# Kernel optimization log

Hardware: AMD Instinct MI355X
Metric: run time of the kernel (lower is better)

The kernel has to match this reference:

```python
import jax, jax.numpy as jnp
import numpy as np

N = 262144   # active voxels
C = 128      # channels (in == out, residual requires it)
K = 27       # 3x3x3 kernel offsets
M = 131072   # kernel-map pairs per offset
EPS = 1e-5


def setup_inputs() -> dict:
    key = jax.random.key(0)
    ks = jax.random.split(key, 10)
    feats = jax.random.normal(ks[0], (N, C), dtype=jnp.float32)
    in_maps = jax.random.randint(ks[1], (K, M), 0, N, dtype=jnp.int32)
    out_maps = jax.random.randint(ks[2], (K, M), 0, N, dtype=jnp.int32)
    # conv weights: one [Cin, Cout] matrix per kernel offset (ME layout), no bias
    W1 = jax.random.normal(ks[3], (K, C, C), dtype=jnp.float32) * (1.0 / np.sqrt(C * K))
    W2 = jax.random.normal(ks[4], (K, C, C), dtype=jnp.float32) * (1.0 / np.sqrt(C * K))
    gamma1 = jnp.ones((C,), jnp.float32)
    beta1 = jnp.zeros((C,), jnp.float32)
    gamma2 = jnp.ones((C,), jnp.float32)
    beta2 = jnp.zeros((C,), jnp.float32)
    return {"feats": feats, "in_maps": in_maps, "out_maps": out_maps,
            "W1": W1, "gamma1": gamma1, "beta1": beta1,
            "W2": W2, "gamma2": gamma2, "beta2": beta2}


def sparse_conv(feats, W, in_maps, out_maps):
    # gather-GEMM-scatter over K=27 kernel offsets (stride 1: N_out == N_in)
    out = jnp.zeros((feats.shape[0], W.shape[2]), feats.dtype)
    for k in range(K):
        gathered = feats[in_maps[k]]          # [M, Cin] irregular gather
        contrib = gathered @ W[k]             # [M, Cout] GEMM
        out = out.at[out_maps[k]].add(contrib)  # scatter-add
    return out


def batch_norm(x, gamma, beta):
    # training-mode BN over the voxel dim with batch stats (biased var)
    mean = jnp.mean(x, axis=0)
    var = jnp.mean(jnp.square(x - mean), axis=0)
    return (x - mean) * jax.lax.rsqrt(var + EPS) * gamma + beta


def reference(feats, in_maps, out_maps, W1, gamma1, beta1, W2, gamma2, beta2):
    out = sparse_conv(feats, W1, in_maps, out_maps)
    out = jax.nn.relu(batch_norm(out, gamma1, beta1))
    out = sparse_conv(out, W2, in_maps, out_maps)
    out = batch_norm(out, gamma2, beta2)
    return jax.nn.relu(out + feats)  # downsample=None -> identity residual
```

## Files before the change

kernel.cpp:

```cpp
#include <hip/hip_runtime.h>
#include <cstdint>

typedef __bf16  bf16x8  __attribute__((ext_vector_type(8)));
typedef short   short8v __attribute__((ext_vector_type(8)));
typedef float   f32x4   __attribute__((ext_vector_type(4)));

constexpr int N  = 262144;
constexpr int C  = 128;
constexpr int K  = 27;
constexpr int M  = 131072;
constexpr int BR = 64;
constexpr int TILES_PER_K = M / BR;

__device__ __forceinline__ uint16_t f2bf(float f) {
    union { float f; uint32_t u; } x; x.f = f;
    uint32_t r = (x.u + 0x7FFFu + ((x.u >> 16) & 1u)) >> 16;
    return (uint16_t)r;
}

__global__ __launch_bounds__(256) void cast_feats_kernel(
    const float* __restrict__ in, uint16_t* __restrict__ out) {
    int i = blockIdx.x * 256 + threadIdx.x;
    const float4* src = reinterpret_cast<const float4*>(in) + (size_t)i * 2;
    float4 a = src[0], b = src[1];
    union { uint16_t u[8]; short8v v; } r;
    r.u[0]=f2bf(a.x); r.u[1]=f2bf(a.y); r.u[2]=f2bf(a.z); r.u[3]=f2bf(a.w);
    r.u[4]=f2bf(b.x); r.u[5]=f2bf(b.y); r.u[6]=f2bf(b.z); r.u[7]=f2bf(b.w);
    *(reinterpret_cast<short8v*>(out) + i) = r.v;
}

__global__ __launch_bounds__(256) void transpose_w_kernel(
    const float* __restrict__ W1, const float* __restrict__ W2,
    uint16_t* __restrict__ WT1, uint16_t* __restrict__ WT2) {
    int i = blockIdx.x * 256 + threadIdx.x;
    int k    = i / (C * C);
    int rem  = i - k * (C * C);
    int cout = rem >> 7;
    int cin  = rem & 127;
    int src  = k * C * C + cin * C + cout;
    WT1[i] = f2bf(W1[src]);
    WT2[i] = f2bf(W2[src]);
}

__global__ __launch_bounds__(256, 3) void conv_kernel(
    const uint16_t* __restrict__ featsB,
    const uint16_t* __restrict__ WT,
    const int* __restrict__ in_maps,
    const int* __restrict__ out_maps,
    float* __restrict__ out)
{
    __shared__ char lds[BR * C * 2 + C * C * 2];
    char* Alds = lds;
    char* Wlds = lds + BR * C * 2;

    const int tile = blockIdx.x;
    const int k    = tile / TILES_PER_K;
    const int m0   = (tile % TILES_PER_K) * BR;
    const int tid  = threadIdx.x;

    {
        const int* im = in_maps + k * M + m0;
        #pragma unroll
        for (int i = 0; i < 4; ++i) {
            int chunk = tid + 256 * i;
            int row   = chunk >> 4;
            int c8    = chunk & 15;
            int g     = im[row];
            short8v v = *reinterpret_cast<const short8v*>(featsB + g * C + c8 * 8);
            int off = (row * 256 + c8 * 16) ^ ((row & 7) << 4);
            *reinterpret_cast<short8v*>(Alds + off) = v;
        }
        const uint16_t* w = WT + k * C * C;
        #pragma unroll
        for (int i = 0; i < 8; ++i) {
            int chunk = tid + 256 * i;
            int cout  = chunk >> 4;
            int c8    = chunk & 15;
            short8v v = *reinterpret_cast<const short8v*>(w + chunk * 8);
            int off = (cout * 256 + c8 * 16) ^ ((cout & 7) << 4);
            *reinterpret_cast<short8v*>(Wlds + off) = v;
        }
    }
    __syncthreads();

    const int wave  = tid >> 6;
    const int lane  = tid & 63;
    const int r16   = lane & 15;
    const int khalf = lane >> 4;

    short8v a[4];
    {
        int row  = wave * 16 + r16;
        int base = row * 256;
        int swz  = (row & 7) << 4;
        #pragma unroll
        for (int kk = 0; kk < 4; ++kk)
            a[kk] = *reinterpret_cast<const short8v*>(Alds + ((base + kk * 64 + khalf * 16) ^ swz));
    }

    f32x4 acc[8];
    #pragma unroll
    for (int t = 0; t < 8; ++t) acc[t] = (f32x4){0.f, 0.f, 0.f, 0.f};

    #pragma unroll
    for (int t = 0; t < 8; ++t) {
        int col  = t * 16 + r16;
        int base = col * 256;
        int swz  = (col & 7) << 4;
        #pragma unroll
        for (int kk = 0; kk < 4; ++kk) {
            short8v b = *reinterpret_cast<const short8v*>(Wlds + ((base + kk * 64 + khalf * 16) ^ swz));
            acc[t] = __builtin_amdgcn_mfma_f32_16x16x32_bf16(
                __builtin_bit_cast(bf16x8, a[kk]), __builtin_bit_cast(bf16x8, b), acc[t], 0, 0, 0);
        }
    }

    const int* om = out_maps + k * M + m0 + wave * 16;
    #pragma unroll
    for (int j = 0; j < 4; ++j) {
        int g = om[khalf * 4 + j];
        float* dst = out + g * C + r16;
        #pragma unroll
        for (int t = 0; t < 8; ++t)
            unsafeAtomicAdd(dst + t * 16, acc[t][j]);
    }
}

__global__ __launch_bounds__(256) void stats_kernel(
    const float* __restrict__ x, float* __restrict__ sums) {
    const int tid = threadIdx.x;
    const int c32 = tid & 31;
    const int rg  = tid >> 5;
    constexpr int RPB = N / 1024;
    float4 s = {0,0,0,0}, q = {0,0,0,0};
    const float* base = x + (size_t)blockIdx.x * RPB * C + c32 * 4;
    for (int r = rg; r < RPB; r += 8) {
        float4 v = *reinterpret_cast<const float4*>(base + r * C);
        s.x += v.x; s.y += v.y; s.z += v.z; s.w += v.w;
        q.x += v.x*v.x; q.y += v.y*v.y; q.z += v.z*v.z; q.w += v.w*v.w;
    }
    __shared__ float4 red[8][32];
    red[rg][c32] = s;
    __syncthreads();
    if (rg == 0) {
        float4 t = red[0][c32];
        #pragma unroll
        for (int j = 1; j < 8; ++j) { float4 u = red[j][c32]; t.x+=u.x; t.y+=u.y; t.z+=u.z; t.w+=u.w; }
        unsafeAtomicAdd(&sums[c32*4+0], t.x); unsafeAtomicAdd(&sums[c32*4+1], t.y);
        unsafeAtomicAdd(&sums[c32*4+2], t.z); unsafeAtomicAdd(&sums[c32*4+3], t.w);
    }
    __syncthreads();
    red[rg][c32] = q;
    __syncthreads();
    if (rg == 0) {
        float4 t = red[0][c32];
        #pragma unroll
        for (int j = 1; j < 8; ++j) { float4 u = red[j][c32]; t.x+=u.x; t.y+=u.y; t.z+=u.z; t.w+=u.w; }
        unsafeAtomicAdd(&sums[C+c32*4+0], t.x); unsafeAtomicAdd(&sums[C+c32*4+1], t.y);
        unsafeAtomicAdd(&sums[C+c32*4+2], t.z); unsafeAtomicAdd(&sums[C+c32*4+3], t.w);
    }
}

__global__ void finalize_kernel(const float* __restrict__ sums,
                                const float* __restrict__ gamma, const float* __restrict__ beta,
                                float* __restrict__ ss) {
    int c = threadIdx.x;
    float m  = sums[c] * (1.0f / N);
    float v  = sums[C + c] * (1.0f / N) - m * m;
    float r  = rsqrtf(v + 1e-5f);
    float sc = gamma[c] * r;
    ss[c]     = sc;
    ss[C + c] = beta[c] - m * sc;
}

__global__ __launch_bounds__(256) void bnrelu_kernel(
    const float* __restrict__ x, const float* __restrict__ ss, uint16_t* __restrict__ out) {
    int i = blockIdx.x * 256 + threadIdx.x;
    int base = i * 8;
    int c = base & 127;
    float4 sc0 = *reinterpret_cast<const float4*>(ss + c);
    float4 sc1 = *reinterpret_cast<const float4*>(ss + c + 4);
    float4 sh0 = *reinterpret_cast<const float4*>(ss + C + c);
    float4 sh1 = *reinterpret_cast<const float4*>(ss + C + c + 4);
    const float4* src = reinterpret_cast<const float4*>(x + base);
    float4 a = src[0], b = src[1];
    union { uint16_t u[8]; short8v v; } r;
    r.u[0] = f2bf(fmaxf(fmaf(a.x, sc0.x, sh0.x), 0.f));
    r.u[1] = f2bf(fmaxf(fmaf(a.y, sc0.y, sh0.y), 0.f));
    r.u[2] = f2bf(fmaxf(fmaf(a.z, sc0.z, sh0.z), 0.f));
    r.u[3] = f2bf(fmaxf(fmaf(a.w, sc0.w, sh0.w), 0.f));
    r.u[4] = f2bf(fmaxf(fmaf(b.x, sc1.x, sh1.x), 0.f));
    r.u[5] = f2bf(fmaxf(fmaf(b.y, sc1.y, sh1.y), 0.f));
    r.u[6] = f2bf(fmaxf(fmaf(b.z, sc1.z, sh1.z), 0.f));
    r.u[7] = f2bf(fmaxf(fmaf(b.w, sc1.w, sh1.w), 0.f));
    *(reinterpret_cast<short8v*>(out) + i) = r.v;
}

__global__ __launch_bounds__(256) void final_kernel(
    float* __restrict__ x, const float* __restrict__ feats, const float* __restrict__ ss) {
    int i = blockIdx.x * 256 + threadIdx.x;
    int base = i * 4;
    int c = base & 127;
    float4 sc = *reinterpret_cast<const float4*>(ss + c);
    float4 sh = *reinterpret_cast<const float4*>(ss + C + c);
    float4 v  = *reinterpret_cast<const float4*>(x + base);
    float4 f  = *reinterpret_cast<const float4*>(feats + base);
    float4 o;
    o.x = fmaxf(fmaf(v.x, sc.x, sh.x) + f.x, 0.f);
    o.y = fmaxf(fmaf(v.y, sc.y, sh.y) + f.y, 0.f);
    o.z = fmaxf(fmaf(v.z, sc.z, sh.z) + f.z, 0.f);
    o.w = fmaxf(fmaf(v.w, sc.w, sh.w) + f.w, 0.f);
    *reinterpret_cast<float4*>(x + base) = o;
}

extern "C" void kernel_launch(void* const* d_in, const int* in_sizes, int n_in,
                              void* d_out, int out_size, void* d_ws, size_t ws_size,
                              hipStream_t stream) {
    const float* feats   = (const float*)d_in[0];
    const int* in_maps   = (const int*)d_in[1];
    const int* out_maps  = (const int*)d_in[2];
    const float* W1      = (const float*)d_in[3];
    const float* gamma1  = (const float*)d_in[4];
    const float* beta1   = (const float*)d_in[5];
    const float* W2      = (const float*)d_in[6];
    const float* gamma2  = (const float*)d_in[7];
    const float* beta2   = (const float*)d_in[8];
    float* out = (float*)d_out;

    char* ws = (char*)d_ws;
    uint16_t* featsB = (uint16_t*)(ws);
    uint16_t* bn1B   = (uint16_t*)(ws + 67108864);
    uint16_t* WT1    = (uint16_t*)(ws + 134217728);
    uint16_t* WT2    = (uint16_t*)(ws + 135102464);
    float*    sums1  = (float*)   (ws + 135987200);
    float*    sums2  = sums1 + 256;
    float*    ss1    = sums1 + 512;
    float*    ss2    = sums1 + 768;

    hipMemsetAsync(out, 0, (size_t)N * C * 4, stream);
    hipMemsetAsync(sums1, 0, 512 * 4, stream);

    cast_feats_kernel<<<N * C / 8 / 256, 256, 0, stream>>>(feats, featsB);
    transpose_w_kernel<<<K * C * C / 256, 256, 0, stream>>>(W1, W2, WT1, WT2);

    conv_kernel<<<K * TILES_PER_K, 256, 0, stream>>>(featsB, WT1, in_maps, out_maps, out);
    stats_kernel<<<1024, 256, 0, stream>>>(out, sums1);
    finalize_kernel<<<1, 128, 0, stream>>>(sums1, gamma1, beta1, ss1);
    bnrelu_kernel<<<N * C / 8 / 256, 256, 0, stream>>>(out, ss1, bn1B);

    hipMemsetAsync(out, 0, (size_t)N * C * 4, stream);
    conv_kernel<<<K * TILES_PER_K, 256, 0, stream>>>(bn1B, WT2, in_maps, out_maps, out);
    stats_kernel<<<1024, 256, 0, stream>>>(out, sums2);
    finalize_kernel<<<1, 128, 0, stream>>>(sums2, gamma2, beta2, ss2);
    final_kernel<<<N * C / 4 / 256, 256, 0, stream>>>(out, feats, ss2);
}
```

Baseline: 3.403 ms.

## Replace atomic scatter-add with output-sorted contributions and segmented reduction

Each convolution's fp32 atomic scatter-add into the output is replaced by a deterministic two-pass scheme. A histogram, a three-kernel prefix scan and a scatter kernel build a CSR-style ordering of all kernel-map pairs by output voxel. The GEMM then writes bf16 contributions directly to their sorted slots, and a reduce kernel sums each voxel's segment into the output. This removes per-element global atomics but adds a roughly 900 MB intermediate buffer plus extra write and read traffic, and rounds each contribution to bf16 before accumulation. The new path runs only when the workspace is large enough; otherwise the old path is kept.

After: 3.395 ms. Within noise of the previous version (-0.2%).

```diff
diff --git a/kernel.cpp b/kernel.cpp
--- a/kernel.cpp
+++ b/kernel.cpp
@@ -9,6 +9,7 @@
 constexpr int C  = 128;
 constexpr int K  = 27;
 constexpr int M  = 131072;
+constexpr int KM = K * M;
 constexpr int BR = 64;
 constexpr int TILES_PER_K = M / BR;
 
@@ -16,6 +17,10 @@
     union { float f; uint32_t u; } x; x.f = f;
     uint32_t r = (x.u + 0x7FFFu + ((x.u >> 16) & 1u)) >> 16;
     return (uint16_t)r;
+}
+__device__ __forceinline__ float bf2f(uint16_t u) {
+    union { uint32_t u; float f; } x; x.u = ((uint32_t)u) << 16;
+    return x.f;
 }
 
 __global__ __launch_bounds__(256) void cast_feats_kernel(
@@ -40,6 +45,173 @@
     int src  = k * C * C + cin * C + cout;
     WT1[i] = f2bf(W1[src]);
     WT2[i] = f2bf(W2[src]);
+}
+
+__global__ __launch_bounds__(256) void hist_kernel(
+    const int* __restrict__ out_maps, int* __restrict__ counts) {
+    int i = blockIdx.x * 256 + threadIdx.x;
+    atomicAdd(&counts[out_maps[i]], 1);
+}
+
+__global__ __launch_bounds__(256) void scan1_kernel(
+    const int* __restrict__ counts, int* __restrict__ row_start, int* __restrict__ bsum) {
+    __shared__ int lds[256];
+    int t = threadIdx.x;
+    int base = blockIdx.x * 1024 + t * 4;
+    int4 c = *reinterpret_cast<const int4*>(counts + base);
+    int tot = c.x + c.y + c.z + c.w;
+    lds[t] = tot;
+    __syncthreads();
+    for (int off = 1; off < 256; off <<= 1) {
+        int v = (t >= off) ? lds[t - off] : 0;
+        __syncthreads();
+        lds[t] += v;
+        __syncthreads();
+    }
+    int excl = lds[t] - tot;
+    int4 o;
+    o.x = excl; o.y = excl + c.x; o.z = o.y + c.y; o.w = o.z + c.z;
+    *reinterpret_cast<int4*>(row_start + base) = o;
+    if (t == 255) bsum[blockIdx.x] = lds[255];
+}
+
+__global__ void scan2_kernel(int* __restrict__ bsum) {
+    __shared__ int lds[256];
+    int t = threadIdx.x;
+    int v0 = bsum[t];
+    lds[t] = v0;
+    __syncthreads();
+    for (int off = 1; off < 256; off <<= 1) {
+        int v = (t >= off) ? lds[t - off] : 0;
+        __syncthreads();
+        lds[t] += v;
+        __syncthreads();
+    }
+    bsum[t] = lds[t] - v0;
+}
+
+__global__ __launch_bounds__(256) void scan3_kernel(
+    int* __restrict__ row_start, const int* __restrict__ bsum) {
+    int i = blockIdx.x * 256 + threadIdx.x;
+    row_start[i] += bsum[i >> 10];
+    if (i == 0) row_start[N] = KM;
+}
+
+__global__ __launch_bounds__(256) void scatter_kernel(
+    const int* __restrict__ out_maps, const int* __restrict__ row_start,
+    int* __restrict__ cursor, int* __restrict__ posArr) {
+    int i = blockIdx.x * 256 + threadIdx.x;
+    int o = out_maps[i];
+    int pos = row_start[o] + atomicAdd(&cursor[o], 1);
+    posArr[i] = pos;
+}
+
+__global__ __launch_bounds__(256, 3) void gemm_kernel(
+    const uint16_t* __restrict__ featsB,
+    const uint16_t* __restrict__ WT,
+    const int* __restrict__ in_maps,
+    const int* __restrict__ posArr,
+    uint16_t* __restrict__ contrib)
+{
+    __shared__ char lds[BR * C * 2 + C * C * 2];
+    char* Alds = lds;
+    char* Wlds = lds + BR * C * 2;
+
+    const int tile = blockIdx.x;
+    const int k    = tile / TILES_PER_K;
+    const int m0   = (tile % TILES_PER_K) * BR;
+    const int tid  = threadIdx.x;
+
+    {
+        const int* im = in_maps + k * M + m0;
+        #pragma unroll
+        for (int i = 0; i < 4; ++i) {
+            int chunk = tid + 256 * i;
+            int row   = chunk >> 4;
+            int c8    = chunk & 15;
+            int g     = im[row];
+            short8v v = *reinterpret_cast<const short8v*>(featsB + (size_t)g * C + c8 * 8);
+            int off = (row * 256 + c8 * 16) ^ ((row & 7) << 4);
+            *reinterpret_cast<short8v*>(Alds + off) = v;
+        }
+        const uint16_t* w = WT + k * C * C;
+        #pragma unroll
+        for (int i = 0; i < 8; ++i) {
+            int chunk = tid + 256 * i;
+            int cout  = chunk >> 4;
+            int c8    = chunk & 15;
+            short8v v = *reinterpret_cast<const short8v*>(w + chunk * 8);
+            int off = (cout * 256 + c8 * 16) ^ ((cout & 7) << 4);
+            *reinterpret_cast<short8v*>(Wlds + off) = v;
+        }
+    }
+    __syncthreads();
+
+    const int wave  = tid >> 6;
+    const int lane  = tid & 63;
+    const int r16   = lane & 15;
+    const int khalf = lane >> 4;
+
+    short8v a[4];
+    {
+        int row  = wave * 16 + r16;
+        int base = row * 256;
+        int swz  = (row & 7) << 4;
+        #pragma unroll
+        for (int kk = 0; kk < 4; ++kk)
+            a[kk] = *reinterpret_cast<const short8v*>(Alds + ((base + kk * 64 + khalf * 16) ^ swz));
+    }
+
+    f32x4 acc[8];
+    #pragma unroll
+    for (int t = 0; t < 8; ++t) acc[t] = (f32x4){0.f, 0.f, 0.f, 0.f};
+
+    #pragma unroll
+    for (int t = 0; t < 8; ++t) {
+        int col  = t * 16 + r16;
+        int base = col * 256;
+        int swz  = (col & 7) << 4;
+        #pragma unroll
+        for (int kk = 0; kk < 4; ++kk) {
+            short8v b = *reinterpret_cast<const short8v*>(Wlds + ((base + kk * 64 + khalf * 16) ^ swz));
+            acc[t] = __builtin_amdgcn_mfma_f32_16x16x32_bf16(
+                __builtin_bit_cast(bf16x8, a[kk]), __builtin_bit_cast(bf16x8, b), acc[t], 0, 0, 0);
+        }
+    }
+
+    const int* pp = posArr + k * M + m0 + wave * 16 + khalf * 4;
+    #pragma unroll
+    for (int j = 0; j < 4; ++j) {
+        int pos = pp[j];
+        uint16_t* dst = contrib + (size_t)pos * C + r16;
+        #pragma unroll
+        for (int t = 0; t < 8; ++t)
+            dst[t * 16] = f2bf(acc[t][j]);
+    }
+}
+
+__global__ __launch_bounds__(256) void reduce_kernel(
+    const uint16_t* __restrict__ contrib, const int* __restrict__ row_start,
+    float* __restrict__ out) {
+    const int tid    = threadIdx.x;
+    const int lane16 = tid & 15;
+    const int grp    = tid >> 4;
+    #pragma unroll
+    for (int rr = 0; rr < 4; ++rr) {
+        int n = blockIdx.x * 64 + rr * 16 + grp;
+        int s = row_start[n], e = row_start[n + 1];
+        float acc[8] = {0.f,0.f,0.f,0.f,0.f,0.f,0.f,0.f};
+        for (int j = s; j < e; ++j) {
+            short8v v = *reinterpret_cast<const short8v*>(contrib + (size_t)j * C + lane16 * 8);
+            #pragma unroll
+            for (int i = 0; i < 8; ++i) acc[i] += bf2f((uint16_t)(unsigned short)v[i]);
+        }
+        float* dst = out + (size_t)n * C + lane16 * 8;
+        float4 o0 = {acc[0], acc[1], acc[2], acc[3]};
+        float4 o1 = {acc[4], acc[5], acc[6], acc[7]};
+        *reinterpret_cast<float4*>(dst)     = o0;
+        *reinterpret_cast<float4*>(dst + 4) = o1;
+    }
 }
 
 __global__ __launch_bounds__(256, 3) void conv_kernel(
@@ -66,7 +238,7 @@
             int row   = chunk >> 4;
             int c8    = chunk & 15;
             int g     = im[row];
-            short8v v = *reinterpret_cast<const short8v*>(featsB + g * C + c8 * 8);
+            short8v v = *reinterpret_cast<const short8v*>(featsB + (size_t)g * C + c8 * 8);
             int off = (row * 256 + c8 * 16) ^ ((row & 7) << 4);
             *reinterpret_cast<short8v*>(Alds + off) = v;
         }
@@ -119,7 +291,7 @@
     #pragma unroll
     for (int j = 0; j < 4; ++j) {
         int g = om[khalf * 4 + j];
-        float* dst = out + g * C + r16;
+        float* dst = out + (size_t)g * C + r16;
         #pragma unroll
         for (int t = 0; t < 8; ++t)
             unsafeAtomicAdd(dst + t * 16, acc[t][j]);
@@ -228,6 +400,64 @@
     float* out = (float*)d_out;
 
     char* ws = (char*)d_ws;
+
+    size_t off = 0;
+    auto alloc = [&](size_t bytes) { size_t o = off; off = (off + bytes + 255) & ~(size_t)255; return o; };
+    size_t o_contrib  = alloc((size_t)KM * C * 2);
+    size_t o_featsB   = alloc((size_t)N * C * 2);
+    size_t o_WT1      = alloc((size_t)K * C * C * 2);
+    size_t o_WT2      = alloc((size_t)K * C * C * 2);
+    size_t o_posArr   = alloc((size_t)KM * 4);
+    size_t o_rowstart = alloc((size_t)(N + 1) * 4);
+    size_t o_counts   = alloc((size_t)N * 4);
+    size_t o_cursor   = alloc((size_t)N * 4);
+    size_t o_bsum     = alloc(1024);
+    size_t o_sums     = alloc(4096);
+    size_t need_fast  = off;
+
+    if (ws_size >= need_fast) {
+        uint16_t* contrib   = (uint16_t*)(ws + o_contrib);
+        uint16_t* featsB    = (uint16_t*)(ws + o_featsB);
+        uint16_t* bn1B      = featsB;
+        uint16_t* WT1       = (uint16_t*)(ws + o_WT1);
+        uint16_t* WT2       = (uint16_t*)(ws + o_WT2);
+        int*      posArr    = (int*)(ws + o_posArr);
+        int*      row_start = (int*)(ws + o_rowstart);
+        int*      counts    = (int*)(ws + o_counts);
+        int*      cursor    = (int*)(ws + o_cursor);
+        int*      bsum      = (int*)(ws + o_bsum);
+        float*    sums1     = (float*)(ws + o_sums);
+        float*    sums2     = sums1 + 256;
+        float*    ss1       = sums1 + 512;
+        float*    ss2       = sums1 + 768;
+
+        hipMemsetAsync(counts, 0, (size_t)N * 4, stream);
+        hipMemsetAsync(cursor, 0, (size_t)N * 4, stream);
+        hipMemsetAsync(sums1, 0, 512 * 4, stream);
+
+        cast_feats_kernel<<<N * C / 8 / 256, 256, 0, stream>>>(feats, featsB);
+        transpose_w_kernel<<<K * C * C / 256, 256, 0, stream>>>(W1, W2, WT1, WT2);
+
+        hist_kernel<<<KM / 256, 256, 0, stream>>>(out_maps, counts);
+        scan1_kernel<<<N / 1024, 256, 0, stream>>>(counts, row_start, bsum);
+        scan2_kernel<<<1, 256, 0, stream>>>(bsum);
+        scan3_kernel<<<N / 256, 256, 0, stream>>>(row_start, bsum);
+        scatter_kernel<<<KM / 256, 256, 0, stream>>>(out_maps, row_start, cursor, posArr);
+
+        gemm_kernel<<<K * TILES_PER_K, 256, 0, stream>>>(featsB, WT1, in_maps, posArr, contrib);
+        reduce_kernel<<<N / 64, 256, 0, stream>>>(contrib, row_start, out);
+        stats_kernel<<<1024, 256, 0, stream>>>(out, sums1);
+        finalize_kernel<<<1, 128, 0, stream>>>(sums1, gamma1, beta1, ss1);
+        bnrelu_kernel<<<N * C / 8 / 256, 256, 0, stream>>>(out, ss1, bn1B);
+
+        gemm_kernel<<<K * TILES_PER_K, 256, 0, stream>>>(bn1B, WT2, in_maps, posArr, contrib);
+        reduce_kernel<<<N / 64, 256, 0, stream>>>(contrib, row_start, out);
+        stats_kernel<<<1024, 256, 0, stream>>>(out, sums2);
+        finalize_kernel<<<1, 128, 0, stream>>>(sums2, gamma2, beta2, ss2);
+        final_kernel<<<N * C / 4 / 256, 256, 0, stream>>>(out, feats, ss2);
+        return;
+    }
+
     uint16_t* featsB = (uint16_t*)(ws);
     uint16_t* bn1B   = (uint16_t*)(ws + 67108864);
     uint16_t* WT1    = (uint16_t*)(ws + 134217728);
```

## Sort kernel map by output row and accumulate convs with packed bf16 atomics

Applied to the files above, without the earlier changes.

Adds a per-offset counting sort (histogram, three-stage scan, scatter) that reorders kernel-map pairs by output row, so each GEMM tile's scatter hits clustered rows. The GEMM epilogue shuffles neighbouring lanes together and issues global_atomic_pk_add_bf16 into a bf16 accumulator, which halves the number of atomics and the bytes they move. Stats, BN-ReLU and the final residual kernel now read that bf16 buffer, and workspace buffers are placed inside d_out. The cost is extra sorting kernels and a 27×N count array in the timed path, and summing about a dozen contributions per element in bf16 may lose enough precision to fail tolerance.

Result: slower. 4.177 ms (+22.7%).

```diff
diff --git a/kernel.cpp b/kernel.cpp
--- a/kernel.cpp
+++ b/kernel.cpp
@@ -9,6 +9,7 @@
 constexpr int C  = 128;
 constexpr int K  = 27;
 constexpr int M  = 131072;
+constexpr int KM = K * M;
 constexpr int BR = 64;
 constexpr int TILES_PER_K = M / BR;
 
@@ -16,6 +17,14 @@
     union { float f; uint32_t u; } x; x.f = f;
     uint32_t r = (x.u + 0x7FFFu + ((x.u >> 16) & 1u)) >> 16;
     return (uint16_t)r;
+}
+__device__ __forceinline__ float bf2f(uint16_t u) {
+    union { uint32_t u; float f; } x; x.u = ((uint32_t)u) << 16;
+    return x.f;
+}
+
+__device__ __forceinline__ void atomic_pk_add_bf16(uint16_t* p, uint32_t v) {
+    asm volatile("global_atomic_pk_add_bf16 %0, %1, off" : : "v"(p), "v"(v) : "memory");
 }
 
 __global__ __launch_bounds__(256) void cast_feats_kernel(
@@ -42,44 +51,108 @@
     WT2[i] = f2bf(W2[src]);
 }
 
-__global__ __launch_bounds__(256, 3) void conv_kernel(
+__global__ __launch_bounds__(256) void hist_kernel(
+    const int* __restrict__ out_maps, int* __restrict__ counts) {
+    int i = blockIdx.x * 256 + threadIdx.x;
+    int k = i >> 17;
+    atomicAdd(&counts[k * N + out_maps[i]], 1);
+}
+
+__global__ __launch_bounds__(256) void scan1_kernel(
+    const int* __restrict__ counts, int* __restrict__ row_start, int* __restrict__ bsum) {
+    __shared__ int lds[256];
+    int t = threadIdx.x;
+    int k   = blockIdx.x >> 8;
+    int blk = blockIdx.x & 255;
+    int base = k * N + blk * 1024 + t * 4;
+    int4 c = *reinterpret_cast<const int4*>(counts + base);
+    int tot = c.x + c.y + c.z + c.w;
+    lds[t] = tot;
+    __syncthreads();
+    for (int off = 1; off < 256; off <<= 1) {
+        int v = (t >= off) ? lds[t - off] : 0;
+        __syncthreads();
+        lds[t] += v;
+        __syncthreads();
+    }
+    int excl = lds[t] - tot;
+    int4 o;
+    o.x = excl; o.y = excl + c.x; o.z = o.y + c.y; o.w = o.z + c.z;
+    *reinterpret_cast<int4*>(row_start + base) = o;
+    if (t == 255) bsum[blockIdx.x] = lds[255];
+}
+
+__global__ void scan2_kernel(int* __restrict__ bsum) {
+    __shared__ int lds[256];
+    int t = threadIdx.x;
+    int base = blockIdx.x * 256 + t;
+    int v0 = bsum[base];
+    lds[t] = v0;
+    __syncthreads();
+    for (int off = 1; off < 256; off <<= 1) {
+        int v = (t >= off) ? lds[t - off] : 0;
+        __syncthreads();
+        lds[t] += v;
+        __syncthreads();
+    }
+    bsum[base] = lds[t] - v0;
+}
+
+__global__ __launch_bounds__(256) void scan3_kernel(
+    int* __restrict__ row_start, const int* __restrict__ bsum) {
+    int i = blockIdx.x * 256 + threadIdx.x;
+    int k   = i >> 18;
+    int win = i & (N - 1);
+    row_start[i] += bsum[(k << 8) + (win >> 10)];
+}
+
+__global__ __launch_bounds__(256) void scatter_kernel(
+    const int* __restrict__ in_maps, const int* __restrict__ out_maps,
+    int* __restrict__ row_start,
+    int2* __restrict__ sInOut) {
+    int i = blockIdx.x * 256 + threadIdx.x;
+    int k = i >> 17;
+    int o = out_maps[i];
+    int pos = atomicAdd(&row_start[k * N + o], 1);
+    int2 v; v.x = in_maps[i]; v.y = o;
+    sInOut[k * M + pos] = v;
+}
+
+__global__ __launch_bounds__(256, 3) void gemm_kernel(
     const uint16_t* __restrict__ featsB,
     const uint16_t* __restrict__ WT,
-    const int* __restrict__ in_maps,
-    const int* __restrict__ out_maps,
-    float* __restrict__ out)
+    const int2* __restrict__ sInOut,
+    uint16_t* __restrict__ outB)
 {
     __shared__ char lds[BR * C * 2 + C * C * 2];
     char* Alds = lds;
     char* Wlds = lds + BR * C * 2;
 
     const int tile = blockIdx.x;
-    const int k    = tile / TILES_PER_K;
-    const int m0   = (tile % TILES_PER_K) * BR;
+    const int k    = tile >> 11;
+    const int m0   = (tile & 2047) * BR;
     const int tid  = threadIdx.x;
-
-    {
-        const int* im = in_maps + k * M + m0;
-        #pragma unroll
-        for (int i = 0; i < 4; ++i) {
-            int chunk = tid + 256 * i;
-            int row   = chunk >> 4;
-            int c8    = chunk & 15;
-            int g     = im[row];
-            short8v v = *reinterpret_cast<const short8v*>(featsB + g * C + c8 * 8);
-            int off = (row * 256 + c8 * 16) ^ ((row & 7) << 4);
-            *reinterpret_cast<short8v*>(Alds + off) = v;
-        }
-        const uint16_t* w = WT + k * C * C;
-        #pragma unroll
-        for (int i = 0; i < 8; ++i) {
-            int chunk = tid + 256 * i;
-            int cout  = chunk >> 4;
-            int c8    = chunk & 15;
-            short8v v = *reinterpret_cast<const short8v*>(w + chunk * 8);
-            int off = (cout * 256 + c8 * 16) ^ ((cout & 7) << 4);
-            *reinterpret_cast<short8v*>(Wlds + off) = v;
-        }
+    const int2* so = sInOut + k * M + m0;
+
+    #pragma unroll
+    for (int i = 0; i < 4; ++i) {
+        int chunk = tid + 256 * i;
+        int row   = chunk >> 4;
+        int c8    = chunk & 15;
+        int g     = so[row].x;
+        short8v v = *reinterpret_cast<const short8v*>(featsB + (size_t)g * C + c8 * 8);
+        int off = (row * 256 + c8 * 16) ^ ((row & 7) << 4);
+        *reinterpret_cast<short8v*>(Alds + off) = v;
+    }
+    const uint16_t* w = WT + k * C * C;
+    #pragma unroll
+    for (int i = 0; i < 8; ++i) {
+        int chunk = tid + 256 * i;
+        int cout  = chunk >> 4;
+        int c8    = chunk & 15;
+        short8v v = *reinterpret_cast<const short8v*>(w + chunk * 8);
+        int off = (cout * 256 + c8 * 16) ^ ((cout & 7) << 4);
+        *reinterpret_cast<short8v*>(Wlds + off) = v;
     }
     __syncthreads();
 
@@ -115,49 +188,68 @@
         }
     }
 
-    const int* om = out_maps + k * M + m0 + wave * 16;
+    const int2* sorow = so + wave * 16 + khalf * 4;
     #pragma unroll
     for (int j = 0; j < 4; ++j) {
-        int g = om[khalf * 4 + j];
-        float* dst = out + g * C + r16;
-        #pragma unroll
-        for (int t = 0; t < 8; ++t)
-            unsafeAtomicAdd(dst + t * 16, acc[t][j]);
+        int orow = sorow[j].y;
+        uint16_t* dst = outB + (size_t)orow * C + r16;
+        #pragma unroll
+        for (int t = 0; t < 8; ++t) {
+            float vlo = acc[t][j];
+            float vhi = __shfl_xor(vlo, 1, 64);
+            if (!(r16 & 1)) {
+                uint32_t pk = (uint32_t)f2bf(vlo) | ((uint32_t)f2bf(vhi) << 16);
+                atomic_pk_add_bf16(dst + t * 16, pk);
+            }
+        }
     }
 }
 
 __global__ __launch_bounds__(256) void stats_kernel(
-    const float* __restrict__ x, float* __restrict__ sums) {
+    const uint16_t* __restrict__ x, float* __restrict__ sums) {
     const int tid = threadIdx.x;
-    const int c32 = tid & 31;
-    const int rg  = tid >> 5;
+    const int cg = tid & 15;
+    const int rg = tid >> 4;
     constexpr int RPB = N / 1024;
-    float4 s = {0,0,0,0}, q = {0,0,0,0};
-    const float* base = x + (size_t)blockIdx.x * RPB * C + c32 * 4;
-    for (int r = rg; r < RPB; r += 8) {
-        float4 v = *reinterpret_cast<const float4*>(base + r * C);
-        s.x += v.x; s.y += v.y; s.z += v.z; s.w += v.w;
-        q.x += v.x*v.x; q.y += v.y*v.y; q.z += v.z*v.z; q.w += v.w*v.w;
-    }
-    __shared__ float4 red[8][32];
-    red[rg][c32] = s;
+    float s[8] = {0,0,0,0,0,0,0,0}, q[8] = {0,0,0,0,0,0,0,0};
+    const uint16_t* base = x + (size_t)blockIdx.x * RPB * C + cg * 8;
+    for (int r = rg; r < RPB; r += 16) {
+        short8v v = *reinterpret_cast<const short8v*>(base + (size_t)r * C);
+        #pragma unroll
+        for (int i = 0; i < 8; ++i) {
+            float f = bf2f((uint16_t)(unsigned short)v[i]);
+            s[i] += f; q[i] += f * f;
+        }
+    }
+    __shared__ float red[16][16][8];
+    #pragma unroll
+    for (int i = 0; i < 8; ++i) red[rg][cg][i] = s[i];
     __syncthreads();
     if (rg == 0) {
-        float4 t = red[0][c32];
-        #pragma unroll
-        for (int j = 1; j < 8; ++j) { float4 u = red[j][c32]; t.x+=u.x; t.y+=u.y; t.z+=u.z; t.w+=u.w; }
-        unsafeAtomicAdd(&sums[c32*4+0], t.x); unsafeAtomicAdd(&sums[c32*4+1], t.y);
-        unsafeAtomicAdd(&sums[c32*4+2], t.z); unsafeAtomicAdd(&sums[c32*4+3], t.w);
-    }
-    __syncthreads();
-    red[rg][c32] = q;
+        float t8[8];
+        #pragma unroll
+        for (int i = 0; i < 8; ++i) t8[i] = red[0][cg][i];
+        #pragma unroll
+        for (int j = 1; j < 16; ++j)
+            #pragma unroll
+            for (int i = 0; i < 8; ++i) t8[i] += red[j][cg][i];
+        #pragma unroll
+        for (int i = 0; i < 8; ++i) unsafeAtomicAdd(&sums[cg * 8 + i], t8[i]);
+    }
+    __syncthreads();
+    #pragma unroll
+    for (int i = 0; i < 8; ++i) red[rg][cg][i] = q[i];
     __syncthreads();
     if (rg == 0) {
-        float4 t = red[0][c32];
-        #pragma unroll
-        for (int j = 1; j < 8; ++j) { float4 u = red[j][c32]; t.x+=u.x; t.y+=u.y; t.z+=u.z; t.w+=u.w; }
-        unsafeAtomicAdd(&sums[C+c32*4+0], t.x); unsafeAtomicAdd(&sums[C+c32*4+1], t.y);
-        unsafeAtomicAdd(&sums[C+c32*4+2], t.z); unsafeAtomicAdd(&sums[C+c32*4+3], t.w);
+        float t8[8];
+        #pragma unroll
+        for (int i = 0; i < 8; ++i) t8[i] = red[0][cg][i];
+        #pragma unroll
+        for (int j = 1; j < 16; ++j)
+            #pragma unroll
+            for (int i = 0; i < 8; ++i) t8[i] += red[j][cg][i];
+        #pragma unroll
+        for (int i = 0; i < 8; ++i) unsafeAtomicAdd(&sums[C + cg * 8 + i], t8[i]);
     }
 }
 
@@ -174,7 +266,7 @@
 }
 
 __global__ __launch_bounds__(256) void bnrelu_kernel(
-    const float* __restrict__ x, const float* __restrict__ ss, uint16_t* __restrict__ out) {
+    const uint16_t* __restrict__ x, const float* __restrict__ ss, uint16_t* __restrict__ out) {
     int i = blockIdx.x * 256 + threadIdx.x;
     int base = i * 8;
     int c = base & 127;
@@ -182,35 +274,49 @@
     float4 sc1 = *reinterpret_cast<const float4*>(ss + c + 4);
     float4 sh0 = *reinterpret_cast<const float4*>(ss + C + c);
     float4 sh1 = *reinterpret_cast<const float4*>(ss + C + c + 4);
-    const float4* src = reinterpret_cast<const float4*>(x + base);
-    float4 a = src[0], b = src[1];
+    short8v v = *reinterpret_cast<const short8v*>(x + base);
+    float f[8];
+    #pragma unroll
+    for (int j = 0; j < 8; ++j) f[j] = bf2f((uint16_t)(unsigned short)v[j]);
     union { uint16_t u[8]; short8v v; } r;
-    r.u[0] = f2bf(fmaxf(fmaf(a.x, sc0.x, sh0.x), 0.f));
-    r.u[1] = f2bf(fmaxf(fmaf(a.y, sc0.y, sh0.y), 0.f));
-    r.u[2] = f2bf(fmaxf(fmaf(a.z, sc0.z, sh0.z), 0.f));
-    r.u[3] = f2bf(fmaxf(fmaf(a.w, sc0.w, sh0.w), 0.f));
-    r.u[4] = f2bf(fmaxf(fmaf(b.x, sc1.x, sh1.x), 0.f));
-    r.u[5] = f2bf(fmaxf(fmaf(b.y, sc1.y, sh1.y), 0.f));
-    r.u[6] = f2bf(fmaxf(fmaf(b.z, sc1.z, sh1.z), 0.f));
-    r.u[7] = f2bf(fmaxf(fmaf(b.w, sc1.w, sh1.w), 0.f));
+    r.u[0] = f2bf(fmaxf(fmaf(f[0], sc0.x, sh0.x), 0.f));
+    r.u[1] = f2bf(fmaxf(fmaf(f[1], sc0.y, sh0.y), 0.f));
+    r.u[2] = f2bf(fmaxf(fmaf(f[2], sc0.z, sh0.z), 0.f));
+    r.u[3] = f2bf(fmaxf(fmaf(f[3], sc0.w, sh0.w), 0.f));
+    r.u[4] = f2bf(fmaxf(fmaf(f[4], sc1.x, sh1.x), 0.f));
+    r.u[5] = f2bf(fmaxf(fmaf(f[5], sc1.y, sh1.y), 0.f));
+    r.u[6] = f2bf(fmaxf(fmaf(f[6], sc1.z, sh1.z), 0.f));
+    r.u[7] = f2bf(fmaxf(fmaf(f[7], sc1.w, sh1.w), 0.f));
     *(reinterpret_cast<short8v*>(out) + i) = r.v;
 }
 
 __global__ __launch_bounds__(256) void final_kernel(
-    float* __restrict__ x, const float* __restrict__ feats, const float* __restrict__ ss) {
-    int i = blockIdx.x * 256 + threadIdx.x;
-    int base = i * 4;
+    const uint16_t* __restrict__ xB, const float* __restrict__ feats,
+    const float* __restrict__ ss, float* __restrict__ out) {
+    int i = blockIdx.x * 256 + threadIdx.x;
+    int base = i * 8;
     int c = base & 127;
-    float4 sc = *reinterpret_cast<const float4*>(ss + c);
-    float4 sh = *reinterpret_cast<const float4*>(ss + C + c);
-    float4 v  = *reinterpret_cast<const float4*>(x + base);
-    float4 f  = *reinterpret_cast<const float4*>(feats + base);
-    float4 o;
-    o.x = fmaxf(fmaf(v.x, sc.x, sh.x) + f.x, 0.f);
-    o.y = fmaxf(fmaf(v.y, sc.y, sh.y) + f.y, 0.f);
-    o.z = fmaxf(fmaf(v.z, sc.z, sh.z) + f.z, 0.f);
-    o.w = fmaxf(fmaf(v.w, sc.w, sh.w) + f.w, 0.f);
-    *reinterpret_cast<float4*>(x + base) = o;
+    float4 sc0 = *reinterpret_cast<const float4*>(ss + c);
+    float4 sc1 = *reinterpret_cast<const float4*>(ss + c + 4);
+    float4 sh0 = *reinterpret_cast<const float4*>(ss + C + c);
+    float4 sh1 = *reinterpret_cast<const float4*>(ss + C + c + 4);
+    short8v v = *reinterpret_cast<const short8v*>(xB + base);
+    float f[8];
+    #pragma unroll
+    for (int j = 0; j < 8; ++j) f[j] = bf2f((uint16_t)(unsigned short)v[j]);
+    const float4* fp = reinterpret_cast<const float4*>(feats + base);
+    float4 r0 = fp[0], r1 = fp[1];
+    float4 o0, o1;
+    o0.x = fmaxf(fmaf(f[0], sc0.x, sh0.x) + r0.x, 0.f);
+    o0.y = fmaxf(fmaf(f[1], sc0.y, sh0.y) + r0.y, 0.f);
+    o0.z = fmaxf(fmaf(f[2], sc0.z, sh0.z) + r0.z, 0.f);
+    o0.w = fmaxf(fmaf(f[3], sc0.w, sh0.w) + r0.w, 0.f);
+    o1.x = fmaxf(fmaf(f[4], sc1.x, sh1.x) + r1.x, 0.f);
+    o1.y = fmaxf(fmaf(f[5], sc1.y, sh1.y) + r1.y, 0.f);
+    o1.z = fmaxf(fmaf(f[6], sc1.z, sh1.z) + r1.z, 0.f);
+    o1.w = fmaxf(fmaf(f[7], sc1.w, sh1.w) + r1.w, 0.f);
+    float4* op = reinterpret_cast<float4*>(out + base);
+    op[0] = o0; op[1] = o1;
 }
 
 extern "C" void kernel_launch(void* const* d_in, const int* in_sizes, int n_in,
@@ -225,32 +331,44 @@
     const float* W2      = (const float*)d_in[6];
     const float* gamma2  = (const float*)d_in[7];
     const float* beta2   = (const float*)d_in[8];
-    float* out = (float*)d_out;
 
     char* ws = (char*)d_ws;
-    uint16_t* featsB = (uint16_t*)(ws);
-    uint16_t* bn1B   = (uint16_t*)(ws + 67108864);
-    uint16_t* WT1    = (uint16_t*)(ws + 134217728);
-    uint16_t* WT2    = (uint16_t*)(ws + 135102464);
-    float*    sums1  = (float*)   (ws + 135987200);
-    float*    sums2  = sums1 + 256;
-    float*    ss1    = sums1 + 512;
-    float*    ss2    = sums1 + 768;
-
-    hipMemsetAsync(out, 0, (size_t)N * C * 4, stream);
+    int2*     sInOut = (int2*)(ws);
+    uint16_t* outB   = (uint16_t*)(ws + 28311552);
+    int*      counts    = (int*)(ws + 28311552);
+    int*      row_start = (int*)(ws + 28311552 + 28311552);
+    uint16_t* WT1   = (uint16_t*)(ws + 95420416);
+    uint16_t* WT2   = (uint16_t*)(ws + 96305152);
+    float*    sums1 = (float*)(ws + 97189888);
+    float*    sums2 = sums1 + 256;
+    float*    ss1   = sums1 + 512;
+    float*    ss2   = sums1 + 768;
+    int*      bsum  = (int*)(ws + 97193984);
+
+    uint16_t* featsB = (uint16_t*)d_out;
+    uint16_t* bn1B   = (uint16_t*)d_out + (size_t)N * C;
+
+    hipMemsetAsync(counts, 0, (size_t)K * N * 4, stream);
     hipMemsetAsync(sums1, 0, 512 * 4, stream);
 
     cast_feats_kernel<<<N * C / 8 / 256, 256, 0, stream>>>(feats, featsB);
     transpose_w_kernel<<<K * C * C / 256, 256, 0, stream>>>(W1, W2, WT1, WT2);
 
-    conv_kernel<<<K * TILES_PER_K, 256, 0, stream>>>(featsB, WT1, in_maps, out_maps, out);
-    stats_kernel<<<1024, 256, 0, stream>>>(out, sums1);
+    hist_kernel<<<KM / 256, 256, 0, stream>>>(out_maps, counts);
+    scan1_kernel<<<K * 256, 256, 0, stream>>>(counts, row_start, bsum);
+    scan2_kernel<<<K, 256, 0, stream>>>(bsum);
+    scan3_kernel<<<K * N / 256, 256, 0, stream>>>(row_start, bsum);
+    scatter_kernel<<<KM / 256, 256, 0, stream>>>(in_maps, out_maps, row_start, sInOut);
+
+    hipMemsetAsync(outB, 0, (size_t)N * C * 2, stream);
+    gemm_kernel<<<K * TILES_PER_K, 256, 0, stream>>>(featsB, WT1, sInOut, outB);
+    stats_kernel<<<1024, 256, 0, stream>>>(outB, sums1);
     finalize_kernel<<<1, 128, 0, stream>>>(sums1, gamma1, beta1, ss1);
-    bnrelu_kernel<<<N * C / 8 / 256, 256, 0, stream>>>(out, ss1, bn1B);
-
-    hipMemsetAsync(out, 0, (size_t)N * C * 4, stream);
-    conv_kernel<<<K * TILES_PER_K, 256, 0, stream>>>(bn1B, WT2, in_maps, out_maps, out);
-    stats_kernel<<<1024, 256, 0, stream>>>(out, sums2);
+    bnrelu_kernel<<<N * C / 8 / 256, 256, 0, stream>>>(outB, ss1, bn1B);
+
+    hipMemsetAsync(outB, 0, (size_t)N * C * 2, stream);
+    gemm_kernel<<<K * TILES_PER_K, 256, 0, stream>>>(bn1B, WT2, sInOut, outB);
+    stats_kernel<<<1024, 256, 0, stream>>>(outB, sums2);
     finalize_kernel<<<1, 128, 0, stream>>>(sums2, gamma2, beta2, ss2);
-    final_kernel<<<N * C / 4 / 256, 256, 0, stream>>>(out, feats, ss2);
-}
+    final_kernel<<<N * C / 8 / 256, 256, 0, stream>>>(outB, feats, ss2, (float*)d_out);
+}
```
